# Kernel tuning notes

Measured on AMD Instinct MI355X. Metric: run time of the kernel, lower is better.

## Reference

```python
import jax, jax.numpy as jnp
import numpy as np

BATCH = 16
N_ROIS = 1000
NUM_CLASSES = 81
DET_MAX = 100
MIN_CONF = 0.7
NMS_THRESH = 0.3
BBOX_STD = jnp.array([0.1, 0.1, 0.2, 0.2], jnp.float32)


def setup_inputs() -> dict:
    key = jax.random.key(0)
    k1, k2, k3, k4, k5 = jax.random.split(key, 5)
    # valid normalized boxes (y1,x1,y2,x2) with y2>y1, x2>x1
    y1 = jax.random.uniform(k1, (BATCH, N_ROIS, 1)) * 0.7
    x1 = jax.random.uniform(k2, (BATCH, N_ROIS, 1)) * 0.7
    hw = jax.random.uniform(k3, (BATCH, N_ROIS, 2)) * 0.28 + 0.02
    rois = jnp.concatenate([y1, x1, y1 + hw[..., :1], x1 + hw[..., 1:]], axis=-1)
    fpn_class = jax.nn.softmax(jax.random.normal(k4, (BATCH, N_ROIS, NUM_CLASSES)) * 2.0, axis=-1)
    fpn_bbox = jax.random.normal(k5, (BATCH, N_ROIS, NUM_CLASSES, 4)) * 0.1
    window = jnp.tile(jnp.array([[0.0, 0.0, 1.0, 1.0]], jnp.float32), (BATCH, 1))
    return {"rois": rois, "fpn_class": fpn_class, "fpn_bbox": fpn_bbox, "window": window}


def apply_box_deltas(boxes, deltas):
    # boxes [N,4] (y1,x1,y2,x2), deltas [N,4] (dy,dx,log dh,log dw)
    h = boxes[:, 2] - boxes[:, 0]
    w = boxes[:, 3] - boxes[:, 1]
    cy = boxes[:, 0] + 0.5 * h
    cx = boxes[:, 1] + 0.5 * w
    cy = cy + deltas[:, 0] * h
    cx = cx + deltas[:, 1] * w
    h = h * jnp.exp(deltas[:, 2])
    w = w * jnp.exp(deltas[:, 3])
    y1 = cy - 0.5 * h
    x1 = cx - 0.5 * w
    return jnp.stack([y1, x1, y1 + h, x1 + w], axis=1)


def clip_boxes(boxes, window):
    wy1, wx1, wy2, wx2 = window[0], window[1], window[2], window[3]
    y1 = jnp.clip(boxes[:, 0], wy1, wy2)
    x1 = jnp.clip(boxes[:, 1], wx1, wx2)
    y2 = jnp.clip(boxes[:, 2], wy1, wy2)
    x2 = jnp.clip(boxes[:, 3], wx1, wx2)
    return jnp.stack([y1, x1, y2, x2], axis=1)


def box_iou(a, b):
    # a [N,4], b [M,4] -> [N,M]
    y1 = jnp.maximum(a[:, None, 0], b[None, :, 0])
    x1 = jnp.maximum(a[:, None, 1], b[None, :, 1])
    y2 = jnp.minimum(a[:, None, 2], b[None, :, 2])
    x2 = jnp.minimum(a[:, None, 3], b[None, :, 3])
    inter = jnp.maximum(y2 - y1, 0.0) * jnp.maximum(x2 - x1, 0.0)
    area_a = (a[:, 2] - a[:, 0]) * (a[:, 3] - a[:, 1])
    area_b = (b[:, 2] - b[:, 0]) * (b[:, 3] - b[:, 1])
    union = area_a[:, None] + area_b[None, :] - inter
    return inter / jnp.maximum(union, 1e-10)


def per_class_nms_mask(boxes, class_ids, scores):
    """boxes [N,4], class_ids [N] int, scores [N] (already -1 where pre-filtered).
    Returns bool [N]: survives greedy per-class NMS (max DET_MAX kept per class)."""
    fg = jnp.arange(1, NUM_CLASSES)                       # [C-1] skip background
    sc = jnp.where(class_ids[None, :] == fg[:, None], scores[None, :], -1.0)  # [C-1,N]
    order = jnp.argsort(-sc, axis=1)                      # [C-1,N] score-desc per class
    iou = box_iou(boxes, boxes)                           # [N,N]
    col = jnp.arange(N_ROIS)
    active0 = sc >= 0.0
    kept0 = jnp.zeros_like(active0)
    cnt0 = jnp.zeros((NUM_CLASSES - 1,), jnp.int32)

    def body(i, carry):
        active, kept, cnt = carry
        cur = order[:, i]                                  # [C-1] current box idx per class
        is_act = jnp.take_along_axis(active, cur[:, None], axis=1)[:, 0]
        is_kept = is_act & (cnt < DET_MAX)
        cnt = cnt + is_kept.astype(jnp.int32)
        kept = kept | ((col[None, :] == cur[:, None]) & is_kept[:, None])
        suppress = is_kept[:, None] & (iou[cur] > NMS_THRESH)  # [C-1,N]
        active = active & ~suppress
        return (active, kept, cnt)

    _, kept, _ = jax.lax.fori_loop(0, N_ROIS, body, (active0, kept0, cnt0))
    return kept.any(axis=0)


def _refine_one(rois, probs, deltas, window):
    n = jnp.arange(N_ROIS)
    class_ids = jnp.argmax(probs, axis=1)                 # [N]
    class_scores = probs[n, class_ids]                    # [N]
    d = deltas[n, class_ids] * BBOX_STD                   # [N,4]
    refined = clip_boxes(apply_box_deltas(rois, d), window)
    keep = (class_ids > 0) & (class_scores >= MIN_CONF)
    sg = jax.lax.stop_gradient
    nms_keep = per_class_nms_mask(
        sg(refined), class_ids, jnp.where(keep, sg(class_scores), -1.0))
    keep = keep & nms_keep
    sf = jnp.where(keep, class_scores, -1.0)
    top_s, top_i = jax.lax.top_k(sf, DET_MAX)             # keep top DET_MAX overall
    valid = top_s >= 0.0
    det = jnp.concatenate(
        [refined[top_i],
         class_ids[top_i][:, None].astype(jnp.float32),
         class_scores[top_i][:, None]], axis=1)           # [DET_MAX,6]
    return jnp.where(valid[:, None], det, 0.0)            # zero-pad invalid rows


def reference(rois, fpn_class, fpn_bbox, window):
    # [B, DET_MAX, 6] = (y1,x1,y2,x2,class_id,score), normalized coords
    return jax.vmap(_refine_one)(rois, fpn_class, fpn_bbox, window)
```

## Files before the change

kernel.cpp:

```cpp
#include <hip/hip_runtime.h>
#include <math.h>

#define BATCH 16
#define N_ROIS 1000
#define NUM_CLASSES 81
#define DET_MAX 100
#define MIN_CONF 0.7f
#define NMS_THRESH 0.3f

#define ROI_TILE 128

__global__ __launch_bounds__(256) void refine_v4(
    const float* __restrict__ rois, const float* __restrict__ probs,
    const float* __restrict__ deltas, const float* __restrict__ window,
    float* __restrict__ ws_box, float* __restrict__ ws_score, int* __restrict__ ws_cls)
{
    __shared__ float s_probs[ROI_TILE * NUM_CLASSES];

    const int base_roi = blockIdx.x * ROI_TILE;

    const float4* src = (const float4*)(probs + (size_t)base_roi * NUM_CLASSES);
    float4* dst = (float4*)s_probs;
    for (int i = threadIdx.x; i < ROI_TILE * NUM_CLASSES / 4; i += 256)
        dst[i] = src[i];
    __syncthreads();

    if (threadIdx.x < ROI_TILE) {
        const int idx = base_roi + threadIdx.x;
        const int b = idx / N_ROIS;

        const float* p = s_probs + threadIdx.x * NUM_CLASSES;
        float bs0 = p[0], bs1 = p[1], bs2 = p[2], bs3 = p[3];
        int ib0 = 0, ib1 = 1, ib2 = 2, ib3 = 3;
        #pragma unroll
        for (int c = 4; c <= 76; c += 4) {
            float v0 = p[c], v1 = p[c + 1], v2 = p[c + 2], v3 = p[c + 3];
            if (v0 > bs0) { bs0 = v0; ib0 = c; }
            if (v1 > bs1) { bs1 = v1; ib1 = c + 1; }
            if (v2 > bs2) { bs2 = v2; ib2 = c + 2; }
            if (v3 > bs3) { bs3 = v3; ib3 = c + 3; }
        }
        { float v = p[80]; if (v > bs0) { bs0 = v; ib0 = 80; } }
        if (bs1 > bs0 || (bs1 == bs0 && ib1 < ib0)) { bs0 = bs1; ib0 = ib1; }
        if (bs3 > bs2 || (bs3 == bs2 && ib3 < ib2)) { bs2 = bs3; ib2 = ib3; }
        if (bs2 > bs0 || (bs2 == bs0 && ib2 < ib0)) { bs0 = bs2; ib0 = ib2; }
        const float bs = bs0;
        const int best = ib0;

        const bool keep = (best > 0) && (bs >= MIN_CONF);
        ws_score[idx] = keep ? bs : -1.0f;

        if (keep) {
            const float4 dd = ((const float4*)deltas)[(size_t)idx * NUM_CLASSES + best];
            float dy = dd.x * 0.1f, dx = dd.y * 0.1f, dh = dd.z * 0.2f, dw = dd.w * 0.2f;

            const float4 rr = ((const float4*)rois)[idx];
            float y1 = rr.x, x1 = rr.y, y2 = rr.z, x2 = rr.w;
            float h = y2 - y1, w = x2 - x1;
            float cy = y1 + 0.5f * h, cx = x1 + 0.5f * w;
            cy += dy * h;
            cx += dx * w;
            h *= expf(dh);
            w *= expf(dw);
            float ny1 = cy - 0.5f * h;
            float nx1 = cx - 0.5f * w;
            float ny2 = ny1 + h;
            float nx2 = nx1 + w;

            const float* win = window + b * 4;
            float wy1 = win[0], wx1 = win[1], wy2 = win[2], wx2 = win[3];
            ny1 = fminf(fmaxf(ny1, wy1), wy2);
            nx1 = fminf(fmaxf(nx1, wx1), wx2);
            ny2 = fminf(fmaxf(ny2, wy1), wy2);
            nx2 = fminf(fmaxf(nx2, wx1), wx2);

            ((float4*)ws_box)[idx] = make_float4(ny1, nx1, ny2, nx2);
            ws_cls[idx] = best;
        }
    }
}

__global__ __launch_bounds__(256) void nms_v4(
    const float* __restrict__ ws_box, const float* __restrict__ ws_score,
    const int* __restrict__ ws_cls, float* __restrict__ out)
{
    const int b = blockIdx.x;
    const int tid = threadIdx.x;

    __shared__ float s_cbox[N_ROIS][4];
    __shared__ float s_csc[N_ROIS];
    __shared__ short s_cidx[N_ROIS];
    __shared__ unsigned char s_ccls[N_ROIS];
    __shared__ float s_sbox[N_ROIS][4];
    __shared__ float s_ssc[N_ROIS];
    __shared__ unsigned char s_scls[N_ROIS];
    __shared__ unsigned char s_kept[N_ROIS];
    __shared__ short s_bucket[N_ROIS];
    __shared__ int s_cnt[NUM_CLASSES];
    __shared__ int s_off[NUM_CLASSES];
    __shared__ int s_C;

    if (tid == 0) s_C = 0;
    if (tid < NUM_CLASSES) s_cnt[tid] = 0;

    for (int i = tid; i < DET_MAX * 6; i += 256)
        out[(size_t)b * DET_MAX * 6 + i] = 0.0f;
    __syncthreads();

    for (int i = tid; i < N_ROIS; i += 256) {
        float sc = ws_score[b * N_ROIS + i];
        if (sc >= 0.0f) {
            int k = atomicAdd(&s_C, 1);
            s_csc[k] = sc;
            s_cidx[k] = (short)i;
            int c = ws_cls[b * N_ROIS + i];
            s_ccls[k] = (unsigned char)c;
            atomicAdd(&s_cnt[c], 1);
            float4 bb = ((const float4*)ws_box)[b * N_ROIS + i];
            s_cbox[k][0] = bb.x; s_cbox[k][1] = bb.y;
            s_cbox[k][2] = bb.z; s_cbox[k][3] = bb.w;
        }
    }
    __syncthreads();
    const int C = s_C;

    if (tid == 0) {
        int acc = 0;
        for (int c = 0; c < NUM_CLASSES; ++c) { s_off[c] = acc; acc += s_cnt[c]; }
    }
    __syncthreads();

    for (int k = tid; k < C; k += 256) {
        float sk = s_csc[k];
        int ik = s_cidx[k];
        int ck = s_ccls[k];
        int rank = 0, crank = 0;
        for (int j = 0; j < C; ++j) {
            float sj = s_csc[j];
            int before = (sj > sk) | ((sj == sk) & (s_cidx[j] < ik));
            rank += before;
            crank += before & (s_ccls[j] == ck);
        }
        s_ssc[rank] = sk;
        s_scls[rank] = (unsigned char)ck;
        s_sbox[rank][0] = s_cbox[k][0];
        s_sbox[rank][1] = s_cbox[k][1];
        s_sbox[rank][2] = s_cbox[k][2];
        s_sbox[rank][3] = s_cbox[k][3];
        s_kept[rank] = 0;
        s_bucket[s_off[ck] + crank] = (short)rank;
    }
    __syncthreads();

    if (tid >= 1 && tid < NUM_CLASSES) {
        const int off = s_off[tid];
        const int m = s_cnt[tid];
        int kept_cnt = 0;
        for (int a = 0; a < m; ++a) {
            if (kept_cnt >= DET_MAX) break;
            int i = s_bucket[off + a];
            float b0 = s_sbox[i][0], b1 = s_sbox[i][1];
            float b2 = s_sbox[i][2], b3 = s_sbox[i][3];
            float area_b = (b2 - b0) * (b3 - b1);
            bool sup = false;
            for (int q = 0; q < a; ++q) {
                int j = s_bucket[off + q];
                if (!s_kept[j]) continue;
                float a0 = s_sbox[j][0], a1 = s_sbox[j][1];
                float a2 = s_sbox[j][2], a3 = s_sbox[j][3];
                float yy1 = fmaxf(a0, b0);
                float xx1 = fmaxf(a1, b1);
                float yy2 = fminf(a2, b2);
                float xx2 = fminf(a3, b3);
                float inter = fmaxf(yy2 - yy1, 0.0f) * fmaxf(xx2 - xx1, 0.0f);
                float area_a = (a2 - a0) * (a3 - a1);
                float uni = area_a + area_b - inter;
                if (inter / fmaxf(uni, 1e-10f) > NMS_THRESH) { sup = true; break; }
            }
            if (!sup) { s_kept[i] = 1; ++kept_cnt; }
        }
    }
    __syncthreads();

    for (int i = tid; i < C; i += 256) {
        if (s_kept[i]) {
            int slot = 0;
            for (int j = 0; j < i; ++j) slot += s_kept[j];
            if (slot < DET_MAX) {
                float* o = out + (size_t)b * DET_MAX * 6 + slot * 6;
                o[0] = s_sbox[i][0];
                o[1] = s_sbox[i][1];
                o[2] = s_sbox[i][2];
                o[3] = s_sbox[i][3];
                o[4] = (float)s_scls[i];
                o[5] = s_ssc[i];
            }
        }
    }
}

extern "C" void kernel_launch(void* const* d_in, const int* in_sizes, int n_in,
                              void* d_out, int out_size, void* d_ws, size_t ws_size,
                              hipStream_t stream) {
    const float* rois      = (const float*)d_in[0];
    const float* fpn_class = (const float*)d_in[1];
    const float* fpn_bbox  = (const float*)d_in[2];
    const float* window    = (const float*)d_in[3];
    float* out = (float*)d_out;

    float* ws_box   = (float*)d_ws;
    float* ws_score = ws_box + (size_t)BATCH * N_ROIS * 4;
    int*   ws_cls   = (int*)(ws_score + (size_t)BATCH * N_ROIS);

    refine_v4<<<BATCH * N_ROIS / ROI_TILE, 256, 0, stream>>>(
        rois, fpn_class, fpn_bbox, window, ws_box, ws_score, ws_cls);
    nms_v4<<<BATCH, 256, 0, stream>>>(ws_box, ws_score, ws_cls, out);
}
```

Baseline: 85.65 us.

## Fuse refine and NMS kernels into one cooperative launch with grid sync

Merges the per-ROI refine kernel and the per-batch NMS kernel into a single cooperative kernel with 128 blocks. The blocks do the refine tiles, then a grid-wide barrier runs, then the first 16 blocks do NMS. Shared memory is reused between the two phases through a union. This removes one kernel launch and the gap between the two kernels, at the cost of a grid barrier and the overhead of a cooperative launch.

Result: slower. 121.4 us (+41.8%).

```diff
diff --git a/kernel.cpp b/kernel.cpp
--- a/kernel.cpp
+++ b/kernel.cpp
@@ -1,5 +1,8 @@
 #include <hip/hip_runtime.h>
+#include <hip/hip_cooperative_groups.h>
 #include <math.h>
+
+namespace cg = cooperative_groups;
 
 #define BATCH 16
 #define N_ROIS 1000
@@ -9,165 +12,175 @@
 #define NMS_THRESH 0.3f
 
 #define ROI_TILE 128
-
-__global__ __launch_bounds__(256) void refine_v4(
+#define N_TILES 125
+#define GRID 128
+
+union SMem {
+    float tile[ROI_TILE * NUM_CLASSES];
+    struct {
+        float cbox[N_ROIS][4];
+        float sbox[N_ROIS][4];
+        float csc[N_ROIS];
+        float ssc[N_ROIS];
+        short cidx[N_ROIS];
+        short bucket[N_ROIS];
+        unsigned char ccls[N_ROIS];
+        unsigned char scls[N_ROIS];
+        unsigned char kept[N_ROIS];
+        int cnt[NUM_CLASSES];
+        int off[NUM_CLASSES];
+        int C;
+    } n;
+};
+
+__global__ __launch_bounds__(256) void detect_coop(
     const float* __restrict__ rois, const float* __restrict__ probs,
     const float* __restrict__ deltas, const float* __restrict__ window,
-    float* __restrict__ ws_box, float* __restrict__ ws_score, int* __restrict__ ws_cls)
+    float* __restrict__ ws_box, float* __restrict__ ws_score,
+    int* __restrict__ ws_cls, float* __restrict__ out)
 {
-    __shared__ float s_probs[ROI_TILE * NUM_CLASSES];
-
-    const int base_roi = blockIdx.x * ROI_TILE;
-
-    const float4* src = (const float4*)(probs + (size_t)base_roi * NUM_CLASSES);
-    float4* dst = (float4*)s_probs;
-    for (int i = threadIdx.x; i < ROI_TILE * NUM_CLASSES / 4; i += 256)
-        dst[i] = src[i];
-    __syncthreads();
-
-    if (threadIdx.x < ROI_TILE) {
-        const int idx = base_roi + threadIdx.x;
-        const int b = idx / N_ROIS;
-
-        const float* p = s_probs + threadIdx.x * NUM_CLASSES;
-        float bs0 = p[0], bs1 = p[1], bs2 = p[2], bs3 = p[3];
-        int ib0 = 0, ib1 = 1, ib2 = 2, ib3 = 3;
-        #pragma unroll
-        for (int c = 4; c <= 76; c += 4) {
-            float v0 = p[c], v1 = p[c + 1], v2 = p[c + 2], v3 = p[c + 3];
-            if (v0 > bs0) { bs0 = v0; ib0 = c; }
-            if (v1 > bs1) { bs1 = v1; ib1 = c + 1; }
-            if (v2 > bs2) { bs2 = v2; ib2 = c + 2; }
-            if (v3 > bs3) { bs3 = v3; ib3 = c + 3; }
-        }
-        { float v = p[80]; if (v > bs0) { bs0 = v; ib0 = 80; } }
-        if (bs1 > bs0 || (bs1 == bs0 && ib1 < ib0)) { bs0 = bs1; ib0 = ib1; }
-        if (bs3 > bs2 || (bs3 == bs2 && ib3 < ib2)) { bs2 = bs3; ib2 = ib3; }
-        if (bs2 > bs0 || (bs2 == bs0 && ib2 < ib0)) { bs0 = bs2; ib0 = ib2; }
-        const float bs = bs0;
-        const int best = ib0;
-
-        const bool keep = (best > 0) && (bs >= MIN_CONF);
-        ws_score[idx] = keep ? bs : -1.0f;
-
-        if (keep) {
-            const float4 dd = ((const float4*)deltas)[(size_t)idx * NUM_CLASSES + best];
-            float dy = dd.x * 0.1f, dx = dd.y * 0.1f, dh = dd.z * 0.2f, dw = dd.w * 0.2f;
-
-            const float4 rr = ((const float4*)rois)[idx];
-            float y1 = rr.x, x1 = rr.y, y2 = rr.z, x2 = rr.w;
-            float h = y2 - y1, w = x2 - x1;
-            float cy = y1 + 0.5f * h, cx = x1 + 0.5f * w;
-            cy += dy * h;
-            cx += dx * w;
-            h *= expf(dh);
-            w *= expf(dw);
-            float ny1 = cy - 0.5f * h;
-            float nx1 = cx - 0.5f * w;
-            float ny2 = ny1 + h;
-            float nx2 = nx1 + w;
-
-            const float* win = window + b * 4;
-            float wy1 = win[0], wx1 = win[1], wy2 = win[2], wx2 = win[3];
-            ny1 = fminf(fmaxf(ny1, wy1), wy2);
-            nx1 = fminf(fmaxf(nx1, wx1), wx2);
-            ny2 = fminf(fmaxf(ny2, wy1), wy2);
-            nx2 = fminf(fmaxf(nx2, wx1), wx2);
-
-            ((float4*)ws_box)[idx] = make_float4(ny1, nx1, ny2, nx2);
-            ws_cls[idx] = best;
-        }
-    }
-}
-
-__global__ __launch_bounds__(256) void nms_v4(
-    const float* __restrict__ ws_box, const float* __restrict__ ws_score,
-    const int* __restrict__ ws_cls, float* __restrict__ out)
-{
-    const int b = blockIdx.x;
+    __shared__ SMem sm;
     const int tid = threadIdx.x;
-
-    __shared__ float s_cbox[N_ROIS][4];
-    __shared__ float s_csc[N_ROIS];
-    __shared__ short s_cidx[N_ROIS];
-    __shared__ unsigned char s_ccls[N_ROIS];
-    __shared__ float s_sbox[N_ROIS][4];
-    __shared__ float s_ssc[N_ROIS];
-    __shared__ unsigned char s_scls[N_ROIS];
-    __shared__ unsigned char s_kept[N_ROIS];
-    __shared__ short s_bucket[N_ROIS];
-    __shared__ int s_cnt[NUM_CLASSES];
-    __shared__ int s_off[NUM_CLASSES];
-    __shared__ int s_C;
-
-    if (tid == 0) s_C = 0;
-    if (tid < NUM_CLASSES) s_cnt[tid] = 0;
-
-    for (int i = tid; i < DET_MAX * 6; i += 256)
-        out[(size_t)b * DET_MAX * 6 + i] = 0.0f;
+    const int blk = blockIdx.x;
+
+    if (blk < N_TILES) {
+        const int base_roi = blk * ROI_TILE;
+
+        const float4* src = (const float4*)(probs + (size_t)base_roi * NUM_CLASSES);
+        float4* dst = (float4*)sm.tile;
+        for (int i = tid; i < ROI_TILE * NUM_CLASSES / 4; i += 256)
+            dst[i] = src[i];
+        __syncthreads();
+
+        if (tid < ROI_TILE) {
+            const int idx = base_roi + tid;
+            const int b = idx / N_ROIS;
+
+            const float* p = sm.tile + tid * NUM_CLASSES;
+            float bs0 = p[0], bs1 = p[1], bs2 = p[2], bs3 = p[3];
+            int ib0 = 0, ib1 = 1, ib2 = 2, ib3 = 3;
+            #pragma unroll
+            for (int c = 4; c <= 76; c += 4) {
+                float v0 = p[c], v1 = p[c + 1], v2 = p[c + 2], v3 = p[c + 3];
+                if (v0 > bs0) { bs0 = v0; ib0 = c; }
+                if (v1 > bs1) { bs1 = v1; ib1 = c + 1; }
+                if (v2 > bs2) { bs2 = v2; ib2 = c + 2; }
+                if (v3 > bs3) { bs3 = v3; ib3 = c + 3; }
+            }
+            { float v = p[80]; if (v > bs0) { bs0 = v; ib0 = 80; } }
+            if (bs1 > bs0 || (bs1 == bs0 && ib1 < ib0)) { bs0 = bs1; ib0 = ib1; }
+            if (bs3 > bs2 || (bs3 == bs2 && ib3 < ib2)) { bs2 = bs3; ib2 = ib3; }
+            if (bs2 > bs0 || (bs2 == bs0 && ib2 < ib0)) { bs0 = bs2; ib0 = ib2; }
+            const float bs = bs0;
+            const int best = ib0;
+
+            const bool keep = (best > 0) && (bs >= MIN_CONF);
+            ws_score[idx] = keep ? bs : -1.0f;
+
+            if (keep) {
+                const float4 dd = ((const float4*)deltas)[(size_t)idx * NUM_CLASSES + best];
+                float dy = dd.x * 0.1f, dx = dd.y * 0.1f, dh = dd.z * 0.2f, dw = dd.w * 0.2f;
+
+                const float4 rr = ((const float4*)rois)[idx];
+                float y1 = rr.x, x1 = rr.y, y2 = rr.z, x2 = rr.w;
+                float h = y2 - y1, w = x2 - x1;
+                float cy = y1 + 0.5f * h, cx = x1 + 0.5f * w;
+                cy += dy * h;
+                cx += dx * w;
+                h *= expf(dh);
+                w *= expf(dw);
+                float ny1 = cy - 0.5f * h;
+                float nx1 = cx - 0.5f * w;
+                float ny2 = ny1 + h;
+                float nx2 = nx1 + w;
+
+                const float* win = window + b * 4;
+                float wy1 = win[0], wx1 = win[1], wy2 = win[2], wx2 = win[3];
+                ny1 = fminf(fmaxf(ny1, wy1), wy2);
+                nx1 = fminf(fmaxf(nx1, wx1), wx2);
+                ny2 = fminf(fmaxf(ny2, wy1), wy2);
+                nx2 = fminf(fmaxf(nx2, wx1), wx2);
+
+                ((float4*)ws_box)[idx] = make_float4(ny1, nx1, ny2, nx2);
+                ws_cls[idx] = best;
+            }
+        }
+    }
+    if (blk < BATCH) {
+        for (int i = tid; i < DET_MAX * 6; i += 256)
+            out[(size_t)blk * DET_MAX * 6 + i] = 0.0f;
+    }
+
+    cg::this_grid().sync();
+
+    if (blk >= BATCH) return;
+    const int b = blk;
+
+    if (tid == 0) sm.n.C = 0;
+    if (tid < NUM_CLASSES) sm.n.cnt[tid] = 0;
     __syncthreads();
 
     for (int i = tid; i < N_ROIS; i += 256) {
         float sc = ws_score[b * N_ROIS + i];
         if (sc >= 0.0f) {
-            int k = atomicAdd(&s_C, 1);
-            s_csc[k] = sc;
-            s_cidx[k] = (short)i;
+            int k = atomicAdd(&sm.n.C, 1);
+            sm.n.csc[k] = sc;
+            sm.n.cidx[k] = (short)i;
             int c = ws_cls[b * N_ROIS + i];
-            s_ccls[k] = (unsigned char)c;
-            atomicAdd(&s_cnt[c], 1);
+            sm.n.ccls[k] = (unsigned char)c;
+            atomicAdd(&sm.n.cnt[c], 1);
             float4 bb = ((const float4*)ws_box)[b * N_ROIS + i];
-            s_cbox[k][0] = bb.x; s_cbox[k][1] = bb.y;
-            s_cbox[k][2] = bb.z; s_cbox[k][3] = bb.w;
-        }
-    }
-    __syncthreads();
-    const int C = s_C;
+            sm.n.cbox[k][0] = bb.x; sm.n.cbox[k][1] = bb.y;
+            sm.n.cbox[k][2] = bb.z; sm.n.cbox[k][3] = bb.w;
+        }
+    }
+    __syncthreads();
+    const int C = sm.n.C;
 
     if (tid == 0) {
         int acc = 0;
-        for (int c = 0; c < NUM_CLASSES; ++c) { s_off[c] = acc; acc += s_cnt[c]; }
+        for (int c = 0; c < NUM_CLASSES; ++c) { sm.n.off[c] = acc; acc += sm.n.cnt[c]; }
     }
     __syncthreads();
 
     for (int k = tid; k < C; k += 256) {
-        float sk = s_csc[k];
-        int ik = s_cidx[k];
-        int ck = s_ccls[k];
+        float sk = sm.n.csc[k];
+        int ik = sm.n.cidx[k];
+        int ck = sm.n.ccls[k];
         int rank = 0, crank = 0;
         for (int j = 0; j < C; ++j) {
-            float sj = s_csc[j];
-            int before = (sj > sk) | ((sj == sk) & (s_cidx[j] < ik));
+            float sj = sm.n.csc[j];
+            int before = (sj > sk) | ((sj == sk) & (sm.n.cidx[j] < ik));
             rank += before;
-            crank += before & (s_ccls[j] == ck);
-        }
-        s_ssc[rank] = sk;
-        s_scls[rank] = (unsigned char)ck;
-        s_sbox[rank][0] = s_cbox[k][0];
-        s_sbox[rank][1] = s_cbox[k][1];
-        s_sbox[rank][2] = s_cbox[k][2];
-        s_sbox[rank][3] = s_cbox[k][3];
-        s_kept[rank] = 0;
-        s_bucket[s_off[ck] + crank] = (short)rank;
+            crank += before & (sm.n.ccls[j] == ck);
+        }
+        sm.n.ssc[rank] = sk;
+        sm.n.scls[rank] = (unsigned char)ck;
+        sm.n.sbox[rank][0] = sm.n.cbox[k][0];
+        sm.n.sbox[rank][1] = sm.n.cbox[k][1];
+        sm.n.sbox[rank][2] = sm.n.cbox[k][2];
+        sm.n.sbox[rank][3] = sm.n.cbox[k][3];
+        sm.n.kept[rank] = 0;
+        sm.n.bucket[sm.n.off[ck] + crank] = (short)rank;
     }
     __syncthreads();
 
     if (tid >= 1 && tid < NUM_CLASSES) {
-        const int off = s_off[tid];
-        const int m = s_cnt[tid];
+        const int off = sm.n.off[tid];
+        const int m = sm.n.cnt[tid];
         int kept_cnt = 0;
         for (int a = 0; a < m; ++a) {
             if (kept_cnt >= DET_MAX) break;
-            int i = s_bucket[off + a];
-            float b0 = s_sbox[i][0], b1 = s_sbox[i][1];
-            float b2 = s_sbox[i][2], b3 = s_sbox[i][3];
+            int i = sm.n.bucket[off + a];
+            float b0 = sm.n.sbox[i][0], b1 = sm.n.sbox[i][1];
+            float b2 = sm.n.sbox[i][2], b3 = sm.n.sbox[i][3];
             float area_b = (b2 - b0) * (b3 - b1);
             bool sup = false;
             for (int q = 0; q < a; ++q) {
-                int j = s_bucket[off + q];
-                if (!s_kept[j]) continue;
-                float a0 = s_sbox[j][0], a1 = s_sbox[j][1];
-                float a2 = s_sbox[j][2], a3 = s_sbox[j][3];
+                int j = sm.n.bucket[off + q];
+                if (!sm.n.kept[j]) continue;
+                float a0 = sm.n.sbox[j][0], a1 = sm.n.sbox[j][1];
+                float a2 = sm.n.sbox[j][2], a3 = sm.n.sbox[j][3];
                 float yy1 = fmaxf(a0, b0);
                 float xx1 = fmaxf(a1, b1);
                 float yy2 = fminf(a2, b2);
@@ -177,23 +190,23 @@
                 float uni = area_a + area_b - inter;
                 if (inter / fmaxf(uni, 1e-10f) > NMS_THRESH) { sup = true; break; }
             }
-            if (!sup) { s_kept[i] = 1; ++kept_cnt; }
+            if (!sup) { sm.n.kept[i] = 1; ++kept_cnt; }
         }
     }
     __syncthreads();
 
     for (int i = tid; i < C; i += 256) {
-        if (s_kept[i]) {
+        if (sm.n.kept[i]) {
             int slot = 0;
-            for (int j = 0; j < i; ++j) slot += s_kept[j];
+            for (int j = 0; j < i; ++j) slot += sm.n.kept[j];
             if (slot < DET_MAX) {
                 float* o = out + (size_t)b * DET_MAX * 6 + slot * 6;
-                o[0] = s_sbox[i][0];
-                o[1] = s_sbox[i][1];
-                o[2] = s_sbox[i][2];
-                o[3] = s_sbox[i][3];
-                o[4] = (float)s_scls[i];
-                o[5] = s_ssc[i];
+                o[0] = sm.n.sbox[i][0];
+                o[1] = sm.n.sbox[i][1];
+                o[2] = sm.n.sbox[i][2];
+                o[3] = sm.n.sbox[i][3];
+                o[4] = (float)sm.n.scls[i];
+                o[5] = sm.n.ssc[i];
             }
         }
     }
@@ -212,7 +225,8 @@
     float* ws_score = ws_box + (size_t)BATCH * N_ROIS * 4;
     int*   ws_cls   = (int*)(ws_score + (size_t)BATCH * N_ROIS);
 
-    refine_v4<<<BATCH * N_ROIS / ROI_TILE, 256, 0, stream>>>(
-        rois, fpn_class, fpn_bbox, window, ws_box, ws_score, ws_cls);
-    nms_v4<<<BATCH, 256, 0, stream>>>(ws_box, ws_score, ws_cls, out);
+    void* args[] = { (void*)&rois, (void*)&fpn_class, (void*)&fpn_bbox, (void*)&window,
+                     (void*)&ws_box, (void*)&ws_score, (void*)&ws_cls, (void*)&out };
+    hipLaunchCooperativeKernel((const void*)detect_coop, dim3(GRID), dim3(256),
+                               args, 0, stream);
 }
```
